# Kernel tuning notes

Measured on AMD Instinct MI355X. Metric: run time of the kernel, lower is better.

The kernel has to match this reference:

```python
import jax, jax.numpy as jnp
import numpy as np

N_NODES = 100000
N_EDGES = 1600000
B_GRAPHS = 64
F_IN = 128
HID = 128
N_CLS = 16
EPS = 1e-5


def setup_inputs() -> dict:
    key = jax.random.key(0)
    ks = jax.random.split(key, 12)
    x = jax.random.normal(ks[0], (N_NODES, F_IN), jnp.float32)
    edge_index = jax.random.randint(ks[1], (2, N_EDGES), 0, N_NODES, dtype=jnp.int32)
    batch = jnp.sort(jax.random.randint(ks[2], (N_NODES,), 0, B_GRAPHS, dtype=jnp.int32))
    sc = lambda fi: 1.0 / np.sqrt(fi)
    return {
        'x': x, 'edge_index': edge_index, 'batch': batch,
        'W1': jax.random.normal(ks[3], (F_IN, HID), jnp.float32) * sc(F_IN),
        'b1': jnp.zeros((HID,), jnp.float32),
        'g1': jnp.ones((HID,), jnp.float32), 'be1': jnp.zeros((HID,), jnp.float32),
        'W2': jax.random.normal(ks[4], (HID, HID), jnp.float32) * sc(HID),
        'b2': jnp.zeros((HID,), jnp.float32),
        'g2': jnp.ones((HID,), jnp.float32), 'be2': jnp.zeros((HID,), jnp.float32),
        'Wg1': jax.random.normal(ks[5], (HID, HID // 2), jnp.float32) * sc(HID),
        'bg1': jnp.zeros((HID // 2,), jnp.float32),
        'Wg2': jax.random.normal(ks[6], (HID // 2, 1), jnp.float32) * sc(HID // 2),
        'bg2': jnp.zeros((1,), jnp.float32),
        'Wc': jax.random.normal(ks[7], (HID, N_CLS), jnp.float32) * sc(HID),
        'bc': jnp.zeros((N_CLS,), jnp.float32),
    }


def gcn_conv(x, src, dst, W, b):
    # GCNConv: h = D^{-1/2}(A+I)D^{-1/2} (x W) + b, self-loops added
    n = x.shape[0]
    h = x @ W
    loop = jnp.arange(n, dtype=src.dtype)
    s = jnp.concatenate([src, loop])
    d = jnp.concatenate([dst, loop])
    deg = jax.ops.segment_sum(jnp.ones_like(d, dtype=h.dtype), d, num_segments=n)
    dinv = jax.lax.rsqrt(deg)  # deg >= 1 thanks to self-loops
    norm = dinv[s] * dinv[d]           # [E+N]
    msg = h[s] * norm[:, None]         # [E+N, HID] gather-transform
    return jax.ops.segment_sum(msg, d, num_segments=n) + b  # scatter-add


def layernorm(x, g, be):
    mu = jnp.mean(x, axis=-1, keepdims=True)
    var = jnp.mean(jnp.square(x - mu), axis=-1, keepdims=True)
    return (x - mu) * jax.lax.rsqrt(var + EPS) * g + be


def att_pool(x, batch, Wg1, bg1, Wg2, bg2, n_graphs):
    gate = jax.nn.relu(x @ Wg1 + bg1) @ Wg2 + bg2           # [N,1]
    gmax = jax.ops.segment_max(gate, batch, num_segments=n_graphs)
    e = jnp.exp(gate - gmax[batch])
    denom = jax.ops.segment_sum(e, batch, num_segments=n_graphs)
    alpha = e / denom[batch]                                 # segment softmax
    return jax.ops.segment_sum(alpha * x, batch, num_segments=n_graphs)


def reference(x, edge_index, batch, W1, b1, g1, be1, W2, b2, g2, be2,
              Wg1, bg1, Wg2, bg2, Wc, bc):
    src, dst = edge_index[0], edge_index[1]
    h = gcn_conv(x, src, dst, W1, b1)
    h = jax.nn.relu(layernorm(h, g1, be1))  # dropout is identity at eval
    h = gcn_conv(h, src, dst, W2, b2)
    h = jax.nn.relu(layernorm(h, g2, be2))
    pooled = att_pool(h, batch, Wg1, bg1, Wg2, bg2, B_GRAPHS)  # [B, HID]
    return pooled @ Wc + bc  # [B, N_CLS]
```

## Files before the change

### kernel.cpp

```cpp
#include <hip/hip_runtime.h>


typedef unsigned short ushort_t;
typedef unsigned int uint_t;
typedef __attribute__((ext_vector_type(8))) short short8;
typedef __attribute__((ext_vector_type(4))) float floatx4;

#define POOL_S 16
#define PAD_DEG 64

__device__ inline ushort_t bf16_rn(float f) {
  uint_t u = __float_as_uint(f);
  u += 0x7fffu + ((u >> 16) & 1u);
  return (ushort_t)(u >> 16);
}
__device__ inline float bf16_lo(uint_t v) { return __uint_as_float(v << 16); }
__device__ inline float bf16_hi(uint_t v) { return __uint_as_float(v & 0xffff0000u); }
__device__ inline uint_t bf16_pack(float a, float b) {
  return (uint_t)bf16_rn(a) | ((uint_t)bf16_rn(b) << 16);
}

__global__ __launch_bounds__(256) void init_kernel(
    int* __restrict__ fill, const float* __restrict__ W1,
    const float* __restrict__ W2, const float* __restrict__ Wg1,
    ushort_t* __restrict__ Wt, uint_t* __restrict__ hs_rowN, int Np) {
  int id = blockIdx.x * 256 + threadIdx.x;
  if (id < Np) { fill[id] = 0; return; }
  int id2 = id - Np;
  if (id2 < 40960) {
    float v;
    if (id2 < 16384) {
      int n = id2 >> 7, k = id2 & 127;
      v = W1[k * 128 + n];
    } else if (id2 < 32768) {
      int i2 = id2 - 16384;
      int n = i2 >> 7, k = i2 & 127;
      v = W2[k * 128 + n];
    } else {
      int i2 = id2 - 32768;
      int n = i2 >> 7, k = i2 & 127;
      v = Wg1[k * 64 + n];
    }
    Wt[id2] = bf16_rn(v);
    return;
  }
  int id3 = id2 - 40960;
  if (id3 < 64) hs_rowN[id3] = 0;
}

template <int TM, int NC, bool IN_F32, bool SCALE, bool BIASRELU, bool GATEDOT>
__device__ __forceinline__ void gemm_tile(
    const void* __restrict__ in, const ushort_t* __restrict__ Wt,
    const float* __restrict__ bias, const float* __restrict__ dinv,
    ushort_t* __restrict__ out, int M, int row0,
    const float* __restrict__ Wg2, const float* __restrict__ bg2,
    float* __restrict__ gate_out, short* As) {
  constexpr int CT = NC / 16;
  constexpr int RT = TM / 64;
  const int t = threadIdx.x;
#pragma unroll
  for (int i = 0; i < TM / 16; ++i) {
    int chunk = t + i * 256;
    int rr = chunk >> 4, c8 = (chunk & 15) * 8;
    int row = row0 + rr;
    short8 val = {0, 0, 0, 0, 0, 0, 0, 0};
    if (IN_F32) {
      const float* inf = (const float*)in;
      if (row < M) {
        float4 v0 = *(const float4*)(inf + (size_t)row * 128 + c8);
        float4 v1 = *(const float4*)(inf + (size_t)row * 128 + c8 + 4);
        val[0] = (short)bf16_rn(v0.x); val[1] = (short)bf16_rn(v0.y);
        val[2] = (short)bf16_rn(v0.z); val[3] = (short)bf16_rn(v0.w);
        val[4] = (short)bf16_rn(v1.x); val[5] = (short)bf16_rn(v1.y);
        val[6] = (short)bf16_rn(v1.z); val[7] = (short)bf16_rn(v1.w);
      }
    } else {
      const short* inb = (const short*)in;
      if (row < M) val = *(const short8*)(inb + (size_t)row * 128 + c8);
    }
    *(short8*)&As[rr * 136 + c8] = val;
  }
  __syncthreads();

  const int wave = t >> 6, lane = t & 63;
  const int m16 = lane & 15, quad = lane >> 4;
  floatx4 acc[RT][CT];
#pragma unroll
  for (int rt = 0; rt < RT; ++rt)
#pragma unroll
    for (int ct = 0; ct < CT; ++ct) acc[rt][ct] = (floatx4){0.f, 0.f, 0.f, 0.f};
#pragma unroll
  for (int ks = 0; ks < 4; ++ks) {
    int koff = ks * 32 + quad * 8;
    short8 a[RT];
#pragma unroll
    for (int rt = 0; rt < RT; ++rt)
      a[rt] = *(const short8*)&As[(wave * 16 + rt * 64 + m16) * 136 + koff];
#pragma unroll
    for (int ct = 0; ct < CT; ++ct) {
      short8 b = *(const short8*)((const short*)Wt + (size_t)(ct * 16 + m16) * 128 + koff);
#pragma unroll
      for (int rt = 0; rt < RT; ++rt)
        acc[rt][ct] = __builtin_amdgcn_mfma_f32_16x16x32_bf16(a[rt], b, acc[rt][ct], 0, 0, 0);
    }
  }

  float bv[CT];
  if (BIASRELU) {
#pragma unroll
    for (int ct = 0; ct < CT; ++ct) bv[ct] = bias[ct * 16 + m16];
  }

  if (GATEDOT) {
    float w2[CT];
#pragma unroll
    for (int ct = 0; ct < CT; ++ct) w2[ct] = Wg2[ct * 16 + m16];
    float bg2v = bg2[0];
#pragma unroll
    for (int rt = 0; rt < RT; ++rt) {
#pragma unroll
      for (int reg = 0; reg < 4; ++reg) {
        float p = 0.f;
#pragma unroll
        for (int ct = 0; ct < CT; ++ct)
          p += fmaxf(acc[rt][ct][reg] + bv[ct], 0.f) * w2[ct];
        p += __shfl_xor(p, 1);
        p += __shfl_xor(p, 2);
        p += __shfl_xor(p, 4);
        p += __shfl_xor(p, 8);
        if (m16 == 0) {
          int row = row0 + wave * 16 + rt * 64 + quad * 4 + reg;
          if (row < M) gate_out[row] = p + bg2v;
        }
      }
    }
    return;
  }

#pragma unroll
  for (int rt = 0; rt < RT; ++rt) {
#pragma unroll
    for (int reg = 0; reg < 4; ++reg) {
      int row = row0 + wave * 16 + rt * 64 + quad * 4 + reg;
      if (row < M) {
        float mult = SCALE ? dinv[row] : 1.f;
#pragma unroll
        for (int ct = 0; ct < CT; ++ct) {
          float v = acc[rt][ct][reg];
          if (BIASRELU) v = fmaxf(v + bv[ct], 0.f);
          else if (SCALE) v *= mult;
          out[(size_t)row * NC + ct * 16 + m16] = bf16_rn(v);
        }
      }
    }
  }
}

__global__ __launch_bounds__(256) void place_gemm1_kernel(
    const int* __restrict__ src, const int* __restrict__ dst,
    int* __restrict__ fill, int* __restrict__ srcs_pad, int E,
    const float* __restrict__ x, const ushort_t* __restrict__ Wt,
    ushort_t* __restrict__ hs, int M, int nPlace, int nGemm) {
  __shared__ short As[64 * 136];
  int b = blockIdx.x;
  int gi = b >> 1;
  if (b & 1) {
    if (gi < nGemm)
      gemm_tile<64, 128, true, false, false, false>(
          x, Wt, nullptr, nullptr, hs, M, gi * 64, nullptr, nullptr, nullptr, As);
    return;
  }
  if (gi < nPlace) {
    int e0 = (gi * 256 + threadIdx.x) * 4;
    if (e0 + 3 < E) {
      int4 d4 = *(const int4*)(dst + e0);
      int4 s4 = *(const int4*)(src + e0);
      int p0 = atomicAdd(&fill[d4.x], 1);
      int p1 = atomicAdd(&fill[d4.y], 1);
      int p2 = atomicAdd(&fill[d4.z], 1);
      int p3 = atomicAdd(&fill[d4.w], 1);
      if (p0 < PAD_DEG) srcs_pad[(size_t)d4.x * PAD_DEG + p0] = s4.x;
      if (p1 < PAD_DEG) srcs_pad[(size_t)d4.y * PAD_DEG + p1] = s4.y;
      if (p2 < PAD_DEG) srcs_pad[(size_t)d4.z * PAD_DEG + p2] = s4.z;
      if (p3 < PAD_DEG) srcs_pad[(size_t)d4.w * PAD_DEG + p3] = s4.w;
    } else {
      for (int j = 0; j < 4; ++j) {
        int e = e0 + j;
        if (e < E) {
          int d = dst[e];
          int pos = atomicAdd(&fill[d], 1);
          if (pos < PAD_DEG) srcs_pad[(size_t)d * PAD_DEG + pos] = src[e];
        }
      }
    }
  }
}

template <int NC, bool SCALE, bool BIASRELU, bool GATEDOT>
__global__ __launch_bounds__(256) void gemm_mfma_kernel(
    const ushort_t* __restrict__ in, const ushort_t* __restrict__ Wt,
    const float* __restrict__ bias, const float* __restrict__ dinv,
    ushort_t* __restrict__ out, int M,
    const float* __restrict__ Wg2, const float* __restrict__ bg2,
    float* __restrict__ gate_out) {
  __shared__ short As[128 * 136];
  gemm_tile<128, NC, false, SCALE, BIASRELU, GATEDOT>(
      in, Wt, bias, dinv, out, M, blockIdx.x * 128, Wg2, bg2, gate_out, As);
}

__device__ __forceinline__ void fma8(float* a, uint4 v, float e) {
  a[0] = fmaf(bf16_lo(v.x), e, a[0]); a[1] = fmaf(bf16_hi(v.x), e, a[1]);
  a[2] = fmaf(bf16_lo(v.y), e, a[2]); a[3] = fmaf(bf16_hi(v.y), e, a[3]);
  a[4] = fmaf(bf16_lo(v.z), e, a[4]); a[5] = fmaf(bf16_hi(v.z), e, a[5]);
  a[6] = fmaf(bf16_lo(v.w), e, a[6]); a[7] = fmaf(bf16_hi(v.w), e, a[7]);
}

template <bool PERSRC>
__global__ __launch_bounds__(256) void aggregate_ln_kernel(
    const ushort_t* __restrict__ hs, const int* __restrict__ fill,
    const int* __restrict__ srcs_pad, float* __restrict__ dinv,
    const float* __restrict__ bias, const float* __restrict__ gamma,
    const float* __restrict__ beta, ushort_t* __restrict__ out, int N) {
  int n = (blockIdx.x * 256 + threadIdx.x) >> 6;
  int lane = threadIdx.x & 63;
  if (n >= N) return;
  const int col = lane & 15, epar = lane >> 4;
  const uint4* hs4 = (const uint4*)hs;
  int sreg = srcs_pad[(size_t)n * PAD_DEG + lane];
  int count = fill[n];
  if (count > PAD_DEG) count = PAD_DEG;
  const int K = (count + 3) & ~3;
  float dv = rsqrtf((float)(count + 1));
  int sc = N;
  float dreg = 0.f;
  if (lane < count) {
    sc = sreg;
    if (PERSRC) dreg = rsqrtf((float)(fill[sc] + 1));
    else        dreg = 1.f;
  }
  float a[8] = {0.f, 0.f, 0.f, 0.f, 0.f, 0.f, 0.f, 0.f};
  int i = epar;
  for (; i + 12 < K; i += 16) {
    int s0 = __shfl(sc, i);       float e0 = __shfl(dreg, i);
    int s1 = __shfl(sc, i + 4);   float e1 = __shfl(dreg, i + 4);
    int s2 = __shfl(sc, i + 8);   float e2 = __shfl(dreg, i + 8);
    int s3 = __shfl(sc, i + 12);  float e3 = __shfl(dreg, i + 12);
    uint4 v0 = hs4[(size_t)s0 * 16 + col];
    uint4 v1 = hs4[(size_t)s1 * 16 + col];
    uint4 v2 = hs4[(size_t)s2 * 16 + col];
    uint4 v3 = hs4[(size_t)s3 * 16 + col];
    fma8(a, v0, e0); fma8(a, v1, e1); fma8(a, v2, e2); fma8(a, v3, e3);
  }
  for (; i < K; i += 4) {
    int s = __shfl(sc, i);
    float e = __shfl(dreg, i);
    uint4 v = hs4[(size_t)s * 16 + col];
    fma8(a, v, e);
  }
#pragma unroll
  for (int k = 0; k < 8; ++k) {
    a[k] += __shfl_xor(a[k], 16);
    a[k] += __shfl_xor(a[k], 32);
  }
  {
    uint4 sv = hs4[(size_t)n * 16 + col];
    fma8(a, sv, PERSRC ? dv : 1.f);
  }
  if (PERSRC && lane == 0) dinv[n] = dv;
  float4 b0 = *(const float4*)(bias + 8 * col);
  float4 b1 = *(const float4*)(bias + 8 * col + 4);
  float y[8];
  y[0] = a[0] * dv + b0.x; y[1] = a[1] * dv + b0.y;
  y[2] = a[2] * dv + b0.z; y[3] = a[3] * dv + b0.w;
  y[4] = a[4] * dv + b1.x; y[5] = a[5] * dv + b1.y;
  y[6] = a[6] * dv + b1.z; y[7] = a[7] * dv + b1.w;
  float s1 = 0.f, s2 = 0.f;
#pragma unroll
  for (int k = 0; k < 8; ++k) { s1 += y[k]; s2 += y[k] * y[k]; }
#pragma unroll
  for (int off = 1; off <= 8; off <<= 1) {
    s1 += __shfl_xor(s1, off);
    s2 += __shfl_xor(s2, off);
  }
  float mu = s1 * (1.f / 128.f);
  float var = s2 * (1.f / 128.f) - mu * mu;
  float rinv = rsqrtf(var + 1e-5f);
  float4 g0 = *(const float4*)(gamma + 8 * col);
  float4 g1 = *(const float4*)(gamma + 8 * col + 4);
  float4 e0 = *(const float4*)(beta + 8 * col);
  float4 e1 = *(const float4*)(beta + 8 * col + 4);
  float o[8];
  o[0] = fmaxf((y[0] - mu) * rinv * g0.x + e0.x, 0.f);
  o[1] = fmaxf((y[1] - mu) * rinv * g0.y + e0.y, 0.f);
  o[2] = fmaxf((y[2] - mu) * rinv * g0.z + e0.z, 0.f);
  o[3] = fmaxf((y[3] - mu) * rinv * g0.w + e0.w, 0.f);
  o[4] = fmaxf((y[4] - mu) * rinv * g1.x + e1.x, 0.f);
  o[5] = fmaxf((y[5] - mu) * rinv * g1.y + e1.y, 0.f);
  o[6] = fmaxf((y[6] - mu) * rinv * g1.z + e1.z, 0.f);
  o[7] = fmaxf((y[7] - mu) * rinv * g1.w + e1.w, 0.f);
  if (epar == 0) {
    uint4 pk;
    pk.x = bf16_pack(o[0], o[1]); pk.y = bf16_pack(o[2], o[3]);
    pk.z = bf16_pack(o[4], o[5]); pk.w = bf16_pack(o[6], o[7]);
    ((uint4*)out)[(size_t)n * 16 + col] = pk;
  }
}

__device__ inline int lower_bound_i(const int* a, int n, int key) {
  int lo = 0, hi = n;
  while (lo < hi) {
    int mid = (lo + hi) >> 1;
    if (a[mid] < key) lo = mid + 1; else hi = mid;
  }
  return lo;
}

__global__ __launch_bounds__(256) void pool_partial_kernel(
    const ushort_t* __restrict__ h2, const float* __restrict__ gate,
    const int* __restrict__ batch, float* __restrict__ partial,
    float2* __restrict__ pstat, int N) {
  int g = blockIdx.x / POOL_S, sub = blockIdx.x % POOL_S;
  int t = threadIdx.x;
  __shared__ float redx[256];
  __shared__ float redy[256];
  __shared__ float s_m;
  int lo = lower_bound_i(batch, N, g);
  int hi = lower_bound_i(batch, N, g + 1);
  int len = hi - lo;
  int chunk = (len + POOL_S - 1) / POOL_S;
  int a = lo + sub * chunk;
  int b = a + chunk < hi ? a + chunk : hi;
  float m = -3.4e38f;
  for (int i = a + t; i < b; i += 256) m = fmaxf(m, gate[i]);
  redx[t] = m;
  __syncthreads();
  for (int off = 128; off; off >>= 1) {
    if (t < off) redx[t] = fmaxf(redx[t], redx[t + off]);
    __syncthreads();
  }
  if (t == 0) s_m = redx[0];
  __syncthreads();
  float gmax = s_m;
  __syncthreads();
  float ssum = 0.f;
  for (int i = a + t; i < b; i += 256) ssum += expf(gate[i] - gmax);
  redx[t] = ssum;
  __syncthreads();
  for (int off = 128; off; off >>= 1) {
    if (t < off) redx[t] += redx[t + off];
    __syncthreads();
  }
  float denom = redx[0];
  __syncthreads();
  int p = t & 63, strm = t >> 6;
  const uint_t* h2u = (const uint_t*)h2;
  float accx = 0.f, accy = 0.f;
  int i = a + strm;
  for (; i + 8 <= b; i += 8) {
    float e0 = expf(gate[i] - gmax);
    float e1 = expf(gate[i + 4] - gmax);
    uint_t v0 = h2u[(size_t)i * 64 + p];
    uint_t v1 = h2u[(size_t)(i + 4) * 64 + p];
    accx += e0 * bf16_lo(v0) + e1 * bf16_lo(v1);
    accy += e0 * bf16_hi(v0) + e1 * bf16_hi(v1);
  }
  for (; i < b; i += 4) {
    float e = expf(gate[i] - gmax);
    uint_t v = h2u[(size_t)i * 64 + p];
    accx += e * bf16_lo(v);
    accy += e * bf16_hi(v);
  }
  redx[t] = accx;
  redy[t] = accy;
  __syncthreads();
  if (t < 64) {
    float px = redx[t] + redx[t + 64] + redx[t + 128] + redx[t + 192];
    float py = redy[t] + redy[t + 64] + redy[t + 128] + redy[t + 192];
    float* dstp = partial + (size_t)blockIdx.x * 128;
    dstp[2 * t] = px;
    dstp[2 * t + 1] = py;
  }
  if (t == 0) pstat[blockIdx.x] = make_float2(gmax, denom);
}

__global__ __launch_bounds__(128) void classify_kernel(
    const float* __restrict__ partial, const float2* __restrict__ pstat,
    const float* __restrict__ Wc, const float* __restrict__ bc,
    float* __restrict__ out) {
  int g = blockIdx.x, t = threadIdx.x;
  __shared__ float pooled[128];
  __shared__ float wgt[POOL_S];
  __shared__ float s_inv;
  if (t == 0) {
    float M = -3.4e38f;
    float2 st[POOL_S];
#pragma unroll
    for (int k = 0; k < POOL_S; ++k) {
      st[k] = pstat[g * POOL_S + k];
      M = fmaxf(M, st[k].x);
    }
    float total = 0.f;
#pragma unroll
    for (int k = 0; k < POOL_S; ++k) {
      float w = expf(st[k].x - M);
      wgt[k] = w;
      total += st[k].y * w;
    }
    s_inv = total > 0.f ? 1.f / total : 0.f;
  }
  __syncthreads();
  float inv = s_inv;
  float s = 0.f;
#pragma unroll
  for (int k = 0; k < POOL_S; ++k)
    s += partial[((size_t)g * POOL_S + k) * 128 + t] * wgt[k];
  pooled[t] = s * inv;
  __syncthreads();
  if (t < 16) {
    float o = bc[t];
    for (int ff = 0; ff < 128; ++ff) o = fmaf(pooled[ff], Wc[ff * 16 + t], o);
    out[g * 16 + t] = o;
  }
}

extern "C" void kernel_launch(void* const* d_in, const int* in_sizes, int n_in,
                              void* d_out, int out_size, void* d_ws, size_t ws_size,
                              hipStream_t stream) {
  const float* x   = (const float*)d_in[0];
  const int*   ei  = (const int*)d_in[1];
  const int*   bat = (const int*)d_in[2];
  const float* W1  = (const float*)d_in[3];
  const float* b1  = (const float*)d_in[4];
  const float* g1  = (const float*)d_in[5];
  const float* be1 = (const float*)d_in[6];
  const float* W2  = (const float*)d_in[7];
  const float* b2  = (const float*)d_in[8];
  const float* g2  = (const float*)d_in[9];
  const float* be2 = (const float*)d_in[10];
  const float* Wg1 = (const float*)d_in[11];
  const float* bg1 = (const float*)d_in[12];
  const float* Wg2 = (const float*)d_in[13];
  const float* bg2 = (const float*)d_in[14];
  const float* Wc  = (const float*)d_in[15];
  const float* bc  = (const float*)d_in[16];

  const int N = in_sizes[0] / 128;
  const int E = in_sizes[1] / 2;
  const int B = out_size / 16;
  const int* src = ei;
  const int* dst = ei + E;

  const int Np = (N + 3) & ~3;

  int* fill      = (int*)d_ws;
  float* dinv    = (float*)(fill + Np);
  float* gatep   = dinv + Np;
  float2* pstat  = (float2*)(gatep + Np);
  float* ppart   = (float*)(pstat + B * POOL_S);
  int* srcs_pad  = (int*)(ppart + (size_t)B * POOL_S * 128);
  ushort_t* Wt   = (ushort_t*)(srcs_pad + (size_t)N * PAD_DEG);
  ushort_t* hs   = Wt + 40960;
  ushort_t* h1   = hs + (size_t)128 * (N + 1);

  const int Pb4 = (E + 1023) / 1024;
  const int Gb64 = (N + 63) / 64;
  const int Gg128 = (N + 127) / 128;

  int initIds = Np + 40960 + 64;
  init_kernel<<<(initIds + 255) / 256, 256, 0, stream>>>(
      fill, W1, W2, Wg1, Wt, (uint_t*)(hs + (size_t)128 * N), Np);

  int nPairs = Pb4 > Gb64 ? Pb4 : Gb64;
  place_gemm1_kernel<<<2 * nPairs, 256, 0, stream>>>(
      src, dst, fill, srcs_pad, E, x, Wt, hs, N, Pb4, Gb64);

  aggregate_ln_kernel<true><<<(N + 3) / 4, 256, 0, stream>>>(
      hs, fill, srcs_pad, dinv, b1, g1, be1, h1, N);
  gemm_mfma_kernel<128, true, false, false><<<Gg128, 256, 0, stream>>>(
      h1, Wt + 16384, nullptr, dinv, hs, N, nullptr, nullptr, nullptr);
  aggregate_ln_kernel<false><<<(N + 3) / 4, 256, 0, stream>>>(
      hs, fill, srcs_pad, dinv, b2, g2, be2, h1, N);
  gemm_mfma_kernel<64, false, true, true><<<Gg128, 256, 0, stream>>>(
      h1, Wt + 32768, bg1, nullptr, nullptr, N, Wg2, bg2, gatep);

  pool_partial_kernel<<<B * POOL_S, 256, 0, stream>>>(
      h1, gatep, bat, ppart, pstat, N);
  classify_kernel<<<B, 128, 0, stream>>>(ppart, pstat, Wc, bc, (float*)d_out);
}
```

Baseline: 387.0 us.

## Replace per-edge global atomics with two-pass bucketed CSR build in shared memory

Edge placement becomes a two-stage counting sort. First each block bins a chunk of edges into coarse destination buckets of 128 nodes, using shared-memory histograms and one global atomic per bucket. Then a build kernel fills each bucket's padded source lists in shared memory and writes them out with coalesced int4 stores. This removes 1.6M scattered global atomics and random writes into the padded adjacency array. In exchange it adds an extra kernel launch and a temporary bucket buffer that reuses h1. Buckets are capped at 4096 entries, so a node range with heavier in-degree would silently drop edges.

```diff
diff --git a/kernel.cpp b/kernel.cpp
--- a/kernel.cpp
+++ b/kernel.cpp
@@ -8,6 +8,11 @@
 
 #define POOL_S 16
 #define PAD_DEG 64
+#define BW_SH 7
+#define BUCKET_W 128
+#define NBMAX 1024
+#define CAP 4096
+#define CHUNK 8192
 
 __device__ inline ushort_t bf16_rn(float f) {
   uint_t u = __float_as_uint(f);
@@ -21,12 +26,12 @@
 }
 
 __global__ __launch_bounds__(256) void init_kernel(
-    int* __restrict__ fill, const float* __restrict__ W1,
+    int* __restrict__ gcount, const float* __restrict__ W1,
     const float* __restrict__ W2, const float* __restrict__ Wg1,
-    ushort_t* __restrict__ Wt, uint_t* __restrict__ hs_rowN, int Np) {
+    ushort_t* __restrict__ Wt, uint_t* __restrict__ hs_rowN) {
   int id = blockIdx.x * 256 + threadIdx.x;
-  if (id < Np) { fill[id] = 0; return; }
-  int id2 = id - Np;
+  if (id < NBMAX) { gcount[id] = 0; return; }
+  int id2 = id - NBMAX;
   if (id2 < 40960) {
     float v;
     if (id2 < 16384) {
@@ -156,12 +161,14 @@
   }
 }
 
-__global__ __launch_bounds__(256) void place_gemm1_kernel(
+__global__ __launch_bounds__(256) void bin_gemm1_kernel(
     const int* __restrict__ src, const int* __restrict__ dst,
-    int* __restrict__ fill, int* __restrict__ srcs_pad, int E,
+    int* __restrict__ gcount, int* __restrict__ buckets, int E,
     const float* __restrict__ x, const ushort_t* __restrict__ Wt,
-    ushort_t* __restrict__ hs, int M, int nPlace, int nGemm) {
+    ushort_t* __restrict__ hs, int M, int nBin, int nGemm) {
   __shared__ short As[64 * 136];
+  __shared__ int cntL[NBMAX];
+  __shared__ int offL[NBMAX];
   int b = blockIdx.x;
   int gi = b >> 1;
   if (b & 1) {
@@ -170,30 +177,62 @@
           x, Wt, nullptr, nullptr, hs, M, gi * 64, nullptr, nullptr, nullptr, As);
     return;
   }
-  if (gi < nPlace) {
-    int e0 = (gi * 256 + threadIdx.x) * 4;
-    if (e0 + 3 < E) {
-      int4 d4 = *(const int4*)(dst + e0);
-      int4 s4 = *(const int4*)(src + e0);
-      int p0 = atomicAdd(&fill[d4.x], 1);
-      int p1 = atomicAdd(&fill[d4.y], 1);
-      int p2 = atomicAdd(&fill[d4.z], 1);
-      int p3 = atomicAdd(&fill[d4.w], 1);
-      if (p0 < PAD_DEG) srcs_pad[(size_t)d4.x * PAD_DEG + p0] = s4.x;
-      if (p1 < PAD_DEG) srcs_pad[(size_t)d4.y * PAD_DEG + p1] = s4.y;
-      if (p2 < PAD_DEG) srcs_pad[(size_t)d4.z * PAD_DEG + p2] = s4.z;
-      if (p3 < PAD_DEG) srcs_pad[(size_t)d4.w * PAD_DEG + p3] = s4.w;
-    } else {
-      for (int j = 0; j < 4; ++j) {
-        int e = e0 + j;
-        if (e < E) {
-          int d = dst[e];
-          int pos = atomicAdd(&fill[d], 1);
-          if (pos < PAD_DEG) srcs_pad[(size_t)d * PAD_DEG + pos] = src[e];
-        }
-      }
-    }
-  }
+  if (gi < nBin) {
+    const int t = threadIdx.x;
+    const int base = gi * CHUNK;
+    int c = E - base;
+    if (c > CHUNK) c = CHUNK;
+    for (int i = t; i < NBMAX; i += 256) cntL[i] = 0;
+    __syncthreads();
+    for (int i = t; i < c; i += 256) {
+      int d = dst[base + i];
+      atomicAdd(&cntL[d >> BW_SH], 1);
+    }
+    __syncthreads();
+    for (int i = t; i < NBMAX; i += 256) {
+      int cn = cntL[i];
+      offL[i] = cn ? atomicAdd(&gcount[i], cn) : 0;
+    }
+    __syncthreads();
+    for (int i = t; i < c; i += 256) {
+      int s = src[base + i];
+      int d = dst[base + i];
+      int bk = d >> BW_SH;
+      int pos = atomicAdd(&offL[bk], 1);
+      if (pos < CAP)
+        buckets[(size_t)bk * CAP + pos] = (s << BW_SH) | (d & (BUCKET_W - 1));
+    }
+  }
+}
+
+__global__ __launch_bounds__(256) void build_kernel(
+    const int* __restrict__ gcount, const int* __restrict__ buckets,
+    int* __restrict__ fill, int* __restrict__ srcs_pad, int N) {
+  __shared__ int fillL[BUCKET_W];
+  __shared__ alignas(16) int srcsL[BUCKET_W * PAD_DEG];
+  const int b = blockIdx.x, t = threadIdx.x;
+  if (t < BUCKET_W) fillL[t] = 0;
+  __syncthreads();
+  int cnt = gcount[b];
+  if (cnt > CAP) cnt = CAP;
+  const int* bk = buckets + (size_t)b * CAP;
+  for (int i = t; i < cnt; i += 256) {
+    int v = bk[i];
+    int local = v & (BUCKET_W - 1);
+    int s = (int)(((uint_t)v) >> BW_SH);
+    int p = atomicAdd(&fillL[local], 1);
+    if (p < PAD_DEG) srcsL[local * PAD_DEG + p] = s;
+  }
+  __syncthreads();
+  const int node0 = b << BW_SH;
+  int width = N - node0;
+  if (width <= 0) return;
+  if (width > BUCKET_W) width = BUCKET_W;
+  if (t < width) fill[node0 + t] = fillL[t];
+  const int tot4 = (width * PAD_DEG) >> 2;
+  int4* dstp = (int4*)(srcs_pad + (size_t)node0 * PAD_DEG);
+  const int4* srcp = (const int4*)srcsL;
+  for (int j = t; j < tot4; j += 256) dstp[j] = srcp[j];
 }
 
 template <int NC, bool SCALE, bool BIASRELU, bool GATEDOT>
@@ -455,24 +494,29 @@
   int* fill      = (int*)d_ws;
   float* dinv    = (float*)(fill + Np);
   float* gatep   = dinv + Np;
-  float2* pstat  = (float2*)(gatep + Np);
+  int* gcount    = (int*)(gatep + Np);
+  float2* pstat  = (float2*)(gcount + NBMAX);
   float* ppart   = (float*)(pstat + B * POOL_S);
   int* srcs_pad  = (int*)(ppart + (size_t)B * POOL_S * 128);
   ushort_t* Wt   = (ushort_t*)(srcs_pad + (size_t)N * PAD_DEG);
   ushort_t* hs   = Wt + 40960;
   ushort_t* h1   = hs + (size_t)128 * (N + 1);
-
-  const int Pb4 = (E + 1023) / 1024;
+  int* buckets   = (int*)h1;
+
+  const int NB = (N + BUCKET_W - 1) >> BW_SH;
+  const int nBin = (E + CHUNK - 1) / CHUNK;
   const int Gb64 = (N + 63) / 64;
   const int Gg128 = (N + 127) / 128;
 
-  int initIds = Np + 40960 + 64;
+  int initIds = NBMAX + 40960 + 64;
   init_kernel<<<(initIds + 255) / 256, 256, 0, stream>>>(
-      fill, W1, W2, Wg1, Wt, (uint_t*)(hs + (size_t)128 * N), Np);
-
-  int nPairs = Pb4 > Gb64 ? Pb4 : Gb64;
-  place_gemm1_kernel<<<2 * nPairs, 256, 0, stream>>>(
-      src, dst, fill, srcs_pad, E, x, Wt, hs, N, Pb4, Gb64);
+      gcount, W1, W2, Wg1, Wt, (uint_t*)(hs + (size_t)128 * N));
+
+  int nPairs = nBin > Gb64 ? nBin : Gb64;
+  bin_gemm1_kernel<<<2 * nPairs, 256, 0, stream>>>(
+      src, dst, gcount, buckets, E, x, Wt, hs, N, nBin, Gb64);
+
+  build_kernel<<<NB, 256, 0, stream>>>(gcount, buckets, fill, srcs_pad, N);
 
   aggregate_ln_kernel<true><<<(N + 3) / 4, 256, 0, stream>>>(
       hs, fill, srcs_pad, dinv, b1, g1, be1, h1, N);
```

Measured after the change: 382.8 us. Within noise of the previous version (-1.1%).
